# Kernel tuning notes

Measured on AMD Instinct MI355X. Metric: run time of the kernel, lower is better.

The kernel has to match this reference:

```python
import jax, jax.numpy as jnp
import numpy as np

N_SIGMA = 1
K_INST = 8  # instance ids 1..K_INST (0 = background)
W_INST, W_VAR, W_SEED = 1.0, 10.0, 1.0
FG_WEIGHT = 1.0


def make_xym(h, w):
    # torch buffer: linspace(0,2,2048) x / linspace(0,1,1024) y, sliced to [0:h,0:w]
    xm = jnp.linspace(0.0, 2.0, 2048)[:w]
    ym = jnp.linspace(0.0, 1.0, 1024)[:h]
    return jnp.stack([jnp.broadcast_to(xm[None, :], (h, w)),
                      jnp.broadcast_to(ym[:, None], (h, w))], axis=0)  # [2,h,w]


def lovasz_hinge_flat(logits, labels):
    # logits, labels: [N] float (labels in {0,1})
    signs = 2.0 * labels - 1.0
    errors = 1.0 - logits * signs
    order = jnp.argsort(-errors)            # descending sort of errors
    errors_sorted = errors[order]
    gt_sorted = labels[order]
    gts = gt_sorted.sum()
    inter = gts - jnp.cumsum(gt_sorted)
    union = gts + jnp.cumsum(1.0 - gt_sorted)
    jac = 1.0 - inter / union
    grad = jnp.concatenate([jac[:1], jac[1:] - jac[:-1]])
    # torch impl wraps grad in Variable() -> no gradient through grad
    return jnp.dot(jax.nn.relu(errors_sorted), jax.lax.stop_gradient(grad))


def spatial_emb_loss(predictions, instances):
    B, C, T, h, w = predictions.shape
    xym = make_xym(h, w)
    # Faithful to the torch source: due to loop indentation, only the last
    # time step's var/instance/seed losses survive, and obj_count == 1.
    pred = predictions[:, :, T - 1]          # [B,C,h,w]
    inst = instances[:, 0, T - 1]            # [B,h,w] int
    spatial_emb = jnp.tanh(pred[:, 0:2]) + xym[None]   # [B,2,h,w]
    sigma = pred[:, 2:2 + N_SIGMA]                     # [B,1,h,w]
    seed = jax.nn.sigmoid(pred[:, 2 + N_SIGMA])        # [B,h,w]
    npix = float(h * w)

    def per_image(se, sig, sd, ins):
        bg_loss = jnp.sum(jnp.where(ins == 0, sd ** 2, 0.0))

        def per_id(k):
            m = (ins == k).astype(se.dtype)            # [h,w]
            cnt = m.sum()
            safe = jnp.maximum(cnt, 1.0)
            # to_center=True: center of in-mask pixel coordinates
            center = jnp.sum(xym * m[None], axis=(1, 2)) / safe      # [2]
            s_mean = jnp.sum(sig * m[None], axis=(1, 2)) / safe      # [n_sigma]
            var_l = jnp.sum(m[None] * (sig - jax.lax.stop_gradient(s_mean)[:, None, None]) ** 2) / (safe * N_SIGMA)
            s_exp = jnp.exp(s_mean * 10.0)
            dist = jnp.exp(-jnp.sum((se - center[:, None, None]) ** 2 * s_exp[:, None, None], axis=0))  # [h,w]
            inst_l = lovasz_hinge_flat((dist * 2.0 - 1.0).reshape(-1), m.reshape(-1))
            seed_l = FG_WEIGHT * jnp.sum(m * (sd - jax.lax.stop_gradient(dist)) ** 2)
            present = (cnt > 0).astype(se.dtype)       # torch skips absent ids
            return present * var_l, present * inst_l, present * seed_l

        var_l, inst_l, seed_l = jax.vmap(per_id)(jnp.arange(1, K_INST + 1))
        seed_loss = (bg_loss + seed_l.sum()) / npix
        # obj_count == 1 in the original code (incremented once per t-loop)
        return W_INST * inst_l.sum() + W_VAR * var_l.sum() + W_SEED * seed_loss

    per_b = jax.vmap(per_image)(spatial_emb, sigma, seed, inst)
    # torch: loss = loss / b, with b == B-1 after the loop
    return per_b.sum() / (B - 1)


def setup_inputs():
    key = jax.random.key(0)
    k1, k2 = jax.random.split(key)
    B, C, T, H, W = 4, 4, 2, 512, 1024
    predictions = jax.random.normal(k1, (B, C, T, H, W), dtype=jnp.float32)
    instances = jax.random.randint(k2, (B, 1, T, H, W), 0, K_INST + 1, dtype=jnp.int32)
    labels = jnp.zeros((B, 1, T, H, W), dtype=jnp.int32)  # unused by forward
    return {"predictions": predictions, "instances": instances, "labels": labels}


def reference(predictions, instances, labels):
    return spatial_emb_loss(predictions, instances)
```

## Files before the change

### kernel.cpp

```cpp
#include <hip/hip_runtime.h>

#define H 512
#define WID 1024
#define HW (H*WID)
#define B 4
#define K 8
#define NB 1024
#define NBLK1 128

#define OFF_LOSS  0
#define OFF_FIN   16
#define OFF_SPART 512
#define OFF_RED   (OFF_SPART + B*K*NBLK1*5)
#define OFF_PART  (OFF_RED + 2*B*K*NB)

static __device__ __forceinline__ float frcp(float x){
#if __has_builtin(__builtin_amdgcn_rcpf)
  return __builtin_amdgcn_rcpf(x);
#else
  return 1.0f / x;
#endif
}
static __device__ __forceinline__ float fexp2(float x){
#if __has_builtin(__builtin_amdgcn_exp2f)
  return __builtin_amdgcn_exp2f(x);
#else
  return exp2f(x);
#endif
}
static __device__ __forceinline__ float ftanh(float x){
  return 1.0f - 2.0f * frcp(__expf(2.0f*x) + 1.0f);
}
static __device__ __forceinline__ float fsigmoid(float x){
  return frcp(1.0f + __expf(-x));
}

__global__ __launch_bounds__(512) void k1_stats(const float* __restrict__ pred,
                                                const int* __restrict__ inst,
                                                float* __restrict__ ws) {
  const int b = blockIdx.y;
  __shared__ int4   ti[1024];
  __shared__ float4 ts[1024];
  __shared__ float  part5[K][5];
  const float4* sig4 = (const float4*)(pred + (size_t)(8*b + 5) * HW);
  const int4*   ins4 = (const int4*)(inst + (size_t)(2*b + 1) * HW);
  const int base4 = blockIdx.x * 1024;
  #pragma unroll
  for (int i = 0; i < 2; i++) {
    const int q = threadIdx.x + i*512;
    ti[q] = ins4[base4 + q];
    ts[q] = sig4[base4 + q];
  }
  __syncthreads();
  const int wv = threadIdx.x >> 6, lane = threadIdx.x & 63;
  const int kk = wv + 1;
  float cnt=0.f, sx=0.f, sy=0.f, ss=0.f, ss2=0.f;
  #pragma unroll
  for (int j = 0; j < 16; j++) {
    const int q = lane + 64*j;
    const int4   iv = ti[q];
    const float4 sv = ts[q];
    const int p = (base4 + q) * 4;
    const float xm0 = (float)(p & (WID-1)) * (2.0f/2047.0f);
    const float ym  = (float)(p >> 10)     * (1.0f/1023.0f);
    const float m0 = (iv.x==kk)?1.f:0.f, m1=(iv.y==kk)?1.f:0.f,
                m2 = (iv.z==kk)?1.f:0.f, m3=(iv.w==kk)?1.f:0.f;
    const float msum = (m0+m1)+(m2+m3);
    cnt += msum;
    sx  += msum*xm0 + (m1 + 2.0f*m2 + 3.0f*m3)*(2.0f/2047.0f);
    sy  += msum*ym;
    ss  += m0*sv.x + m1*sv.y + m2*sv.z + m3*sv.w;
    ss2 += m0*sv.x*sv.x + m1*sv.y*sv.y + m2*sv.z*sv.z + m3*sv.w*sv.w;
  }
  #pragma unroll
  for (int o=1;o<64;o<<=1){
    cnt+=__shfl_xor(cnt,o,64);
    sx +=__shfl_xor(sx, o,64);
    sy +=__shfl_xor(sy, o,64);
    ss +=__shfl_xor(ss, o,64);
    ss2+=__shfl_xor(ss2,o,64);
  }
  if (lane == 0) {
    part5[wv][0]=cnt; part5[wv][1]=sx; part5[wv][2]=sy; part5[wv][3]=ss; part5[wv][4]=ss2;
  }
  __syncthreads();
  if (threadIdx.x < K*5) {
    const int w = threadIdx.x / 5, c = threadIdx.x % 5;
    ws[OFF_SPART + ((size_t)(b*K + w)*NBLK1 + blockIdx.x)*5 + c] = part5[w][c];
  }
}

__global__ __launch_bounds__(256) void k2_fin(float* __restrict__ ws) {
  const int t = threadIdx.x;
  const int bk = t >> 3, s = t & 7;
  float a0=0.f,a1=0.f,a2=0.f,a3=0.f,a4=0.f;
  for (int j = 0; j < NBLK1/8; j++) {
    const float* p = ws + OFF_SPART + ((size_t)bk*NBLK1 + (s + 8*j))*5;
    a0+=p[0]; a1+=p[1]; a2+=p[2]; a3+=p[3]; a4+=p[4];
  }
  #pragma unroll
  for (int o=1;o<8;o<<=1){
    a0+=__shfl_xor(a0,o,64); a1+=__shfl_xor(a1,o,64); a2+=__shfl_xor(a2,o,64);
    a3+=__shfl_xor(a3,o,64); a4+=__shfl_xor(a4,o,64);
  }
  __shared__ float vloc[32];
  if (s == 0) {
    const float cnt=a0, sx=a1, sy=a2, ss=a3, ss2=a4;
    const float present = (cnt > 0.0f) ? 1.0f : 0.0f;
    const float safe = fmaxf(cnt, 1.0f);
    const float cx = sx/safe, cy = sy/safe, sm = ss/safe;
    const float var = (ss2 - 2.0f*sm*ss + sm*sm*cnt)/safe;
    const float sexp = expf(10.0f * sm);
    const float L2E = 1.4426950408889634f;
    float* fin = ws + OFF_FIN + bk*8;
    fin[0] = -sexp*L2E;
    fin[1] =  2.0f*sexp*cx*L2E;
    fin[2] =  2.0f*sexp*cy*L2E;
    fin[3] = -sexp*(cx*cx + cy*cy)*L2E + 10.0f;
    fin[4] = cnt;
    vloc[bk] = present * 10.0f * var * (1.0f/3.0f);
  }
  __syncthreads();
  if (t == 0) {
    float v = 0.f;
    #pragma unroll
    for (int i = 0; i < 32; i++) v += vloc[i];
    atomicAdd(ws + OFF_LOSS, v);
  }
}

template<int G>
__global__ __launch_bounds__(256) void k3_main(const float* __restrict__ pred,
                                               const int* __restrict__ inst,
                                               float* __restrict__ ws,
                                               unsigned int* __restrict__ part) {
  const int b = blockIdx.y, g = blockIdx.x;
  __shared__ unsigned int hist[K*NB];
  for (int i = threadIdx.x; i < K*NB; i += 256) hist[i] = 0;
  float4 fr[K];
  #pragma unroll
  for (int k=0;k<K;k++){
    const float* fin = ws + OFF_FIN + (b*K + k)*8;
    fr[k] = make_float4(fin[0], fin[1], fin[2], fin[3]);
  }
  __syncthreads();
  const float4* p0 = (const float4*)(pred + (size_t)(8*b+1)*HW);
  const float4* p1 = (const float4*)(pred + (size_t)(8*b+3)*HW);
  const float4* p3 = (const float4*)(pred + (size_t)(8*b+7)*HW);
  const int4*   in4 = (const int4*)(inst + (size_t)(2*b+1)*HW);
  float sAcc = 0.0f;
  constexpr int CH4 = HW / (G*4);
  const int base4 = g * CH4;
  #pragma unroll
  for (int q0 = 0; q0 < CH4; q0 += 256) {
    const int idx = base4 + q0 + threadIdx.x;
    const int4   iv = in4[idx];
    const float4 f0 = p0[idx];
    const float4 f1 = p1[idx];
    const float4 f3 = p3[idx];
    const int p = idx * 4;
    const float xm0 = (float)(p & (WID-1)) * (2.0f/2047.0f);
    const float ym  = (float)(p >> 10)     * (1.0f/1023.0f);
    const int   ivv[4] = {iv.x, iv.y, iv.z, iv.w};
    const float a0v[4] = {f0.x, f0.y, f0.z, f0.w};
    const float a1v[4] = {f1.x, f1.y, f1.z, f1.w};
    const float a3v[4] = {f3.x, f3.y, f3.z, f3.w};
    #pragma unroll
    for (int e4 = 0; e4 < 4; e4++) {
      const int ivp = ivv[e4];
      const float px = ftanh(a0v[e4]) + xm0 + (float)e4*(2.0f/2047.0f);
      const float py = ftanh(a1v[e4]) + ym;
      const float sd = fsigmoid(a3v[e4]);
      const float t2 = px*px + py*py;
      float down = 0.0f;
      #pragma unroll
      for (int j=0;j<K;j++){
        const float u = fmaf(fr[j].x, t2, fmaf(fr[j].y, px, fmaf(fr[j].z, py, fr[j].w)));
        const float v = fexp2(u);
        int vi = (int)v; vi = (vi > NB-1) ? NB-1 : vi;
        const bool own = (ivp == j+1);
        const int bu = own ? (NB-1 - vi) : vi;
        if (own) down = v;
        atomicAdd(&hist[j*NB + bu], own ? 0x10001u : 1u);
      }
      const float d  = (ivp == 0) ? 0.0f : down * (1.0f/1024.0f);
      const float df = sd - d;
      sAcc += df*df;
    }
  }
  __syncthreads();
  unsigned int* dst = part + ((size_t)b*G + g)*(K*NB);
  for (int i = threadIdx.x; i < K*NB; i += 256) dst[i] = hist[i];
  #pragma unroll
  for (int o=1;o<64;o<<=1) sAcc += __shfl_xor(sAcc, o, 64);
  __shared__ float wsum[4];
  if ((threadIdx.x & 63) == 0) wsum[threadIdx.x>>6] = sAcc;
  __syncthreads();
  if (threadIdx.x == 0) {
    const float tot = wsum[0]+wsum[1]+wsum[2]+wsum[3];
    atomicAdd(ws + OFF_LOSS, tot * (1.0f/((float)HW * 3.0f)));
  }
}

__global__ __launch_bounds__(128) void k4a_reduce(const unsigned int* __restrict__ part,
                                                  unsigned int* __restrict__ red, int G) {
  const int bk = blockIdx.x, c = blockIdx.y;
  const int b = bk >> 3, k = bk & 7;
  const int bu = c*128 + threadIdx.x;
  const unsigned int* base = part + (size_t)b*G*K*NB + (size_t)k*NB + bu;
  unsigned int rc = 0, rp = 0;
  #pragma unroll 4
  for (int g = 0; g < G; g++) {
    const unsigned int v = base[(size_t)g*K*NB];
    rc += v & 0xFFFFu;
    rp += v >> 16;
  }
  red[bk*NB + bu]            = rc;
  red[B*K*NB + bk*NB + bu]   = rp;
}

__global__ __launch_bounds__(256) void k4b_lovasz(const unsigned int* __restrict__ red,
                                                   float* __restrict__ ws) {
  const int bk = blockIdx.x;
  const float cntF = ws[OFF_FIN + bk*8 + 4];
  if (cntF <= 0.0f) return;
  const double Pd = (double)cntF;
  const int t = threadIdx.x;
  const int lane = t & 63, wv = t >> 6;
  unsigned int cnt[4], pos[4];
  #pragma unroll
  for (int j = 0; j < 4; j++) {
    const int bu = NB-1 - (t*4 + j);
    cnt[j] = red[bk*NB + bu];
    pos[j] = red[B*K*NB + bk*NB + bu];
  }
  const int lc = (int)(cnt[0]+cnt[1]+cnt[2]+cnt[3]);
  const int lp = (int)(pos[0]+pos[1]+pos[2]+pos[3]);
  int ic = lc, ip = lp;
  #pragma unroll
  for (int o=1;o<64;o<<=1){
    const int vc = __shfl_up(ic, o, 64);
    const int vp = __shfl_up(ip, o, 64);
    if (lane >= o) { ic += vc; ip += vp; }
  }
  __shared__ int wtc[4], wtp[4];
  if (lane == 63) { wtc[wv] = ic; wtp[wv] = ip; }
  __syncthreads();
  int offc = 0, offp = 0;
  for (int w = 0; w < wv; w++) { offc += wtc[w]; offp += wtp[w]; }
  int irun = offc + ic - lc;
  int crun = offp + ip - lp;
  double acc = 0.0;
  #pragma unroll
  for (int j = 0; j < 4; j++) {
    const int n = (int)cnt[j];
    if (n) {
      const int bu = NB-1 - (t*4 + j);
      const double jac0 = (irun==0) ? 0.0 : 1.0 - (Pd - crun)/(Pd + irun - crun);
      irun += n; crun += (int)pos[j];
      const double jac1 = 1.0 - (Pd - crun)/(Pd + irun - crun);
      acc += ((bu + 0.5) * (2.0/NB)) * (jac1 - jac0);
    }
  }
  #pragma unroll
  for (int o=1;o<64;o<<=1) acc += __shfl_xor(acc, o, 64);
  __shared__ double racc[4];
  if (lane == 0) racc[wv] = acc;
  __syncthreads();
  if (t == 0) {
    const double tot = racc[0]+racc[1]+racc[2]+racc[3];
    atomicAdd(ws + OFF_LOSS, (float)(tot * (1.0/3.0)));
  }
}

__global__ void k5_out(const float* __restrict__ ws, float* __restrict__ out) {
  if (threadIdx.x == 0) out[0] = ws[OFF_LOSS];
}

extern "C" void kernel_launch(void* const* d_in, const int* in_sizes, int n_in,
                              void* d_out, int out_size, void* d_ws, size_t ws_size,
                              hipStream_t stream) {
  const float* pred = (const float*)d_in[0];
  const int*   inst = (const int*)d_in[1];
  float* ws  = (float*)d_ws;
  float* out = (float*)d_out;
  unsigned int* red  = ((unsigned int*)d_ws) + OFF_RED;
  unsigned int* part = ((unsigned int*)d_ws) + OFF_PART;
  int G = 128;
  while (G > 32 && ws_size < ((size_t)OFF_PART + (size_t)B*G*K*NB)*4) G >>= 1;
  hipMemsetAsync(d_ws, 0, (size_t)OFF_FIN*4 + 64, stream);
  k1_stats<<<dim3(NBLK1,B), 512, 0, stream>>>(pred, inst, ws);
  k2_fin  <<<1, 256, 0, stream>>>(ws);
  if      (G == 128) k3_main<128><<<dim3(128,B), 256, 0, stream>>>(pred, inst, ws, part);
  else if (G ==  64) k3_main< 64><<<dim3( 64,B), 256, 0, stream>>>(pred, inst, ws, part);
  else               k3_main< 32><<<dim3( 32,B), 256, 0, stream>>>(pred, inst, ws, part);
  k4a_reduce<<<dim3(B*K, 8), 128, 0, stream>>>(part, red, G);
  k4b_lovasz<<<B*K, 256, 0, stream>>>(red, ws);
  k5_out  <<<1, 64, 0, stream>>>(ws, out);
}
```

Baseline: 141.8 us.

## Fuse stats finalize, histogram reduce, and output into fewer kernels via last-block counters

```diff
diff --git a/kernel.cpp b/kernel.cpp
--- a/kernel.cpp
+++ b/kernel.cpp
@@ -7,12 +7,14 @@
 #define K 8
 #define NB 1024
 #define NBLK1 128
+#define G3 64
 
 #define OFF_LOSS  0
+#define OFF_CTRA  8
+#define OFF_CTRC  9
 #define OFF_FIN   16
 #define OFF_SPART 512
-#define OFF_RED   (OFF_SPART + B*K*NBLK1*5)
-#define OFF_PART  (OFF_RED + 2*B*K*NB)
+#define OFF_PART  (OFF_SPART + B*K*NBLK1*5)
 
 static __device__ __forceinline__ float frcp(float x){
 #if __has_builtin(__builtin_amdgcn_rcpf)
@@ -35,9 +37,10 @@
   return frcp(1.0f + __expf(-x));
 }
 
-__global__ __launch_bounds__(512) void k1_stats(const float* __restrict__ pred,
+__global__ __launch_bounds__(512) void kA_stats(const float* __restrict__ pred,
                                                 const int* __restrict__ inst,
-                                                float* __restrict__ ws) {
+                                                float* __restrict__ ws,
+                                                unsigned int* __restrict__ ctr) {
   const int b = blockIdx.y;
   __shared__ int4   ti[1024];
   __shared__ float4 ts[1024];
@@ -88,28 +91,33 @@
     const int w = threadIdx.x / 5, c = threadIdx.x % 5;
     ws[OFF_SPART + ((size_t)(b*K + w)*NBLK1 + blockIdx.x)*5 + c] = part5[w][c];
   }
-}
-
-__global__ __launch_bounds__(256) void k2_fin(float* __restrict__ ws) {
+  __threadfence();
+  __shared__ int lastB;
+  if (threadIdx.x == 0)
+    lastB = (atomicAdd(ctr, 1u) == (unsigned)(NBLK1*B - 1)) ? 1 : 0;
+  __syncthreads();
+  if (!lastB) return;
+  __threadfence();
   const int t = threadIdx.x;
-  const int bk = t >> 3, s = t & 7;
+  const int bk = t >> 4, s = t & 15;
   float a0=0.f,a1=0.f,a2=0.f,a3=0.f,a4=0.f;
-  for (int j = 0; j < NBLK1/8; j++) {
-    const float* p = ws + OFF_SPART + ((size_t)bk*NBLK1 + (s + 8*j))*5;
+  #pragma unroll
+  for (int j = 0; j < NBLK1/16; j++) {
+    const float* p = ws + OFF_SPART + ((size_t)bk*NBLK1 + (s + 16*j))*5;
     a0+=p[0]; a1+=p[1]; a2+=p[2]; a3+=p[3]; a4+=p[4];
   }
   #pragma unroll
-  for (int o=1;o<8;o<<=1){
+  for (int o=1;o<16;o<<=1){
     a0+=__shfl_xor(a0,o,64); a1+=__shfl_xor(a1,o,64); a2+=__shfl_xor(a2,o,64);
     a3+=__shfl_xor(a3,o,64); a4+=__shfl_xor(a4,o,64);
   }
   __shared__ float vloc[32];
   if (s == 0) {
-    const float cnt=a0, sx=a1, sy=a2, ss=a3, ss2=a4;
-    const float present = (cnt > 0.0f) ? 1.0f : 0.0f;
-    const float safe = fmaxf(cnt, 1.0f);
-    const float cx = sx/safe, cy = sy/safe, sm = ss/safe;
-    const float var = (ss2 - 2.0f*sm*ss + sm*sm*cnt)/safe;
+    const float cntT=a0, sx2=a1, sy2=a2, ss1=a3, ss21=a4;
+    const float present = (cntT > 0.0f) ? 1.0f : 0.0f;
+    const float safe = fmaxf(cntT, 1.0f);
+    const float cx = sx2/safe, cy = sy2/safe, sm = ss1/safe;
+    const float var = (ss21 - 2.0f*sm*ss1 + sm*sm*cntT)/safe;
     const float sexp = expf(10.0f * sm);
     const float L2E = 1.4426950408889634f;
     float* fin = ws + OFF_FIN + bk*8;
@@ -117,7 +125,7 @@
     fin[1] =  2.0f*sexp*cx*L2E;
     fin[2] =  2.0f*sexp*cy*L2E;
     fin[3] = -sexp*(cx*cx + cy*cy)*L2E + 10.0f;
-    fin[4] = cnt;
+    fin[4] = cntT;
     vloc[bk] = present * 10.0f * var * (1.0f/3.0f);
   }
   __syncthreads();
@@ -125,12 +133,11 @@
     float v = 0.f;
     #pragma unroll
     for (int i = 0; i < 32; i++) v += vloc[i];
-    atomicAdd(ws + OFF_LOSS, v);
-  }
-}
-
-template<int G>
-__global__ __launch_bounds__(256) void k3_main(const float* __restrict__ pred,
+    ws[OFF_LOSS] = v;
+  }
+}
+
+__global__ __launch_bounds__(256) void kB_main(const float* __restrict__ pred,
                                                const int* __restrict__ inst,
                                                float* __restrict__ ws,
                                                unsigned int* __restrict__ part) {
@@ -149,7 +156,7 @@
   const float4* p3 = (const float4*)(pred + (size_t)(8*b+7)*HW);
   const int4*   in4 = (const int4*)(inst + (size_t)(2*b+1)*HW);
   float sAcc = 0.0f;
-  constexpr int CH4 = HW / (G*4);
+  constexpr int CH4 = HW / (G3*4);
   const int base4 = g * CH4;
   #pragma unroll
   for (int q0 = 0; q0 < CH4; q0 += 256) {
@@ -189,7 +196,7 @@
     }
   }
   __syncthreads();
-  unsigned int* dst = part + ((size_t)b*G + g)*(K*NB);
+  unsigned int* dst = part + ((size_t)b*G3 + g)*(K*NB);
   for (int i = threadIdx.x; i < K*NB; i += 256) dst[i] = hist[i];
   #pragma unroll
   for (int o=1;o<64;o<<=1) sAcc += __shfl_xor(sAcc, o, 64);
@@ -202,40 +209,25 @@
   }
 }
 
-__global__ __launch_bounds__(128) void k4a_reduce(const unsigned int* __restrict__ part,
-                                                  unsigned int* __restrict__ red, int G) {
-  const int bk = blockIdx.x, c = blockIdx.y;
+__global__ __launch_bounds__(512) void kC_lovasz(const unsigned int* __restrict__ part,
+                                                 float* __restrict__ ws,
+                                                 float* __restrict__ out,
+                                                 unsigned int* __restrict__ ctr) {
+  const int bk = blockIdx.x;
   const int b = bk >> 3, k = bk & 7;
-  const int bu = c*128 + threadIdx.x;
-  const unsigned int* base = part + (size_t)b*G*K*NB + (size_t)k*NB + bu;
-  unsigned int rc = 0, rp = 0;
+  const int t = threadIdx.x, lane = t & 63, wv = t >> 6;
+  const int bu0 = NB-1 - 2*t, bu1 = bu0 - 1;
+  const unsigned int* base = part + (size_t)b*G3*K*NB + (size_t)k*NB;
+  unsigned int c0=0,pz0=0,c1=0,pz1=0;
   #pragma unroll 4
-  for (int g = 0; g < G; g++) {
-    const unsigned int v = base[(size_t)g*K*NB];
-    rc += v & 0xFFFFu;
-    rp += v >> 16;
-  }
-  red[bk*NB + bu]            = rc;
-  red[B*K*NB + bk*NB + bu]   = rp;
-}
-
-__global__ __launch_bounds__(256) void k4b_lovasz(const unsigned int* __restrict__ red,
-                                                   float* __restrict__ ws) {
-  const int bk = blockIdx.x;
+  for (int g = 0; g < G3; g++) {
+    const unsigned int v0 = base[(size_t)g*K*NB + bu0];
+    const unsigned int v1 = base[(size_t)g*K*NB + bu1];
+    c0 += v0 & 0xFFFFu;  pz0 += v0 >> 16;
+    c1 += v1 & 0xFFFFu;  pz1 += v1 >> 16;
+  }
   const float cntF = ws[OFF_FIN + bk*8 + 4];
-  if (cntF <= 0.0f) return;
-  const double Pd = (double)cntF;
-  const int t = threadIdx.x;
-  const int lane = t & 63, wv = t >> 6;
-  unsigned int cnt[4], pos[4];
-  #pragma unroll
-  for (int j = 0; j < 4; j++) {
-    const int bu = NB-1 - (t*4 + j);
-    cnt[j] = red[bk*NB + bu];
-    pos[j] = red[B*K*NB + bk*NB + bu];
-  }
-  const int lc = (int)(cnt[0]+cnt[1]+cnt[2]+cnt[3]);
-  const int lp = (int)(pos[0]+pos[1]+pos[2]+pos[3]);
+  const int lc = (int)(c0 + c1), lp = (int)(pz0 + pz1);
   int ic = lc, ip = lp;
   #pragma unroll
   for (int o=1;o<64;o<<=1){
@@ -243,7 +235,7 @@
     const int vp = __shfl_up(ip, o, 64);
     if (lane >= o) { ic += vc; ip += vp; }
   }
-  __shared__ int wtc[4], wtp[4];
+  __shared__ int wtc[8], wtp[8];
   if (lane == 63) { wtc[wv] = ic; wtp[wv] = ip; }
   __syncthreads();
   int offc = 0, offp = 0;
@@ -251,30 +243,40 @@
   int irun = offc + ic - lc;
   int crun = offp + ip - lp;
   double acc = 0.0;
-  #pragma unroll
-  for (int j = 0; j < 4; j++) {
-    const int n = (int)cnt[j];
-    if (n) {
-      const int bu = NB-1 - (t*4 + j);
+  if (cntF > 0.0f) {
+    const double Pd = (double)cntF;
+    if (c0) {
       const double jac0 = (irun==0) ? 0.0 : 1.0 - (Pd - crun)/(Pd + irun - crun);
-      irun += n; crun += (int)pos[j];
+      irun += (int)c0; crun += (int)pz0;
       const double jac1 = 1.0 - (Pd - crun)/(Pd + irun - crun);
-      acc += ((bu + 0.5) * (2.0/NB)) * (jac1 - jac0);
+      acc += ((bu0 + 0.5) * (2.0/NB)) * (jac1 - jac0);
+    } else irun += (int)c0;
+    if (c1) {
+      const double jac0 = (irun==0) ? 0.0 : 1.0 - (Pd - crun)/(Pd + irun - crun);
+      irun += (int)c1; crun += (int)pz1;
+      const double jac1 = 1.0 - (Pd - crun)/(Pd + irun - crun);
+      acc += ((bu1 + 0.5) * (2.0/NB)) * (jac1 - jac0);
     }
   }
   #pragma unroll
   for (int o=1;o<64;o<<=1) acc += __shfl_xor(acc, o, 64);
-  __shared__ double racc[4];
+  __shared__ double racc[8];
   if (lane == 0) racc[wv] = acc;
   __syncthreads();
   if (t == 0) {
-    const double tot = racc[0]+racc[1]+racc[2]+racc[3];
+    double tot = 0.0;
+    #pragma unroll
+    for (int i = 0; i < 8; i++) tot += racc[i];
     atomicAdd(ws + OFF_LOSS, (float)(tot * (1.0/3.0)));
   }
-}
-
-__global__ void k5_out(const float* __restrict__ ws, float* __restrict__ out) {
-  if (threadIdx.x == 0) out[0] = ws[OFF_LOSS];
+  __threadfence();
+  __shared__ int lastB;
+  if (t == 0) lastB = (atomicAdd(ctr, 1u) == (unsigned)(B*K - 1)) ? 1 : 0;
+  __syncthreads();
+  if (lastB && t == 0) {
+    __threadfence();
+    out[0] = atomicAdd(ws + OFF_LOSS, 0.0f);
+  }
 }
 
 extern "C" void kernel_launch(void* const* d_in, const int* in_sizes, int n_in,
@@ -284,17 +286,11 @@
   const int*   inst = (const int*)d_in[1];
   float* ws  = (float*)d_ws;
   float* out = (float*)d_out;
-  unsigned int* red  = ((unsigned int*)d_ws) + OFF_RED;
+  unsigned int* ctrA = ((unsigned int*)d_ws) + OFF_CTRA;
+  unsigned int* ctrC = ((unsigned int*)d_ws) + OFF_CTRC;
   unsigned int* part = ((unsigned int*)d_ws) + OFF_PART;
-  int G = 128;
-  while (G > 32 && ws_size < ((size_t)OFF_PART + (size_t)B*G*K*NB)*4) G >>= 1;
-  hipMemsetAsync(d_ws, 0, (size_t)OFF_FIN*4 + 64, stream);
-  k1_stats<<<dim3(NBLK1,B), 512, 0, stream>>>(pred, inst, ws);
-  k2_fin  <<<1, 256, 0, stream>>>(ws);
-  if      (G == 128) k3_main<128><<<dim3(128,B), 256, 0, stream>>>(pred, inst, ws, part);
-  else if (G ==  64) k3_main< 64><<<dim3( 64,B), 256, 0, stream>>>(pred, inst, ws, part);
-  else               k3_main< 32><<<dim3( 32,B), 256, 0, stream>>>(pred, inst, ws, part);
-  k4a_reduce<<<dim3(B*K, 8), 128, 0, stream>>>(part, red, G);
-  k4b_lovasz<<<B*K, 256, 0, stream>>>(red, ws);
-  k5_out  <<<1, 64, 0, stream>>>(ws, out);
-}
+  hipMemsetAsync(d_ws, 0, 2048, stream);
+  kA_stats<<<dim3(NBLK1,B), 512, 0, stream>>>(pred, inst, ws, ctrA);
+  kB_main <<<dim3(G3,B),   256, 0, stream>>>(pred, inst, ws, part);
+  kC_lovasz<<<B*K,         512, 0, stream>>>(part, ws, out, ctrC);
+}
```

Result: slower. 206.2 us (+45.3%).
